# Kernel tuning notes

Measured on AMD Instinct MI355X. Metric: run time of the kernel, lower is better.

## Reference

```python
import jax, jax.numpy as jnp
from jax import lax
import numpy as np

B, N1, N2 = 4, 2048, 8192
C1, C2, K, F = 128, 64, 15, 128
NSAMPLE = 16
RADIUS = 0.2
KP_EXTEND = 1.0
EXTENT = KP_EXTEND * RADIUS  # area of influence of each kernel point


def setup_inputs() -> dict:
    key = jax.random.key(0)
    k0, k1, k2, k3, k4 = jax.random.split(key, 5)
    xyz1 = jax.random.uniform(k0, (B, N1, 3), dtype=jnp.float32)
    xyz2 = jax.random.uniform(k1, (B, N2, 3), dtype=jnp.float32)
    features1 = jax.random.normal(k2, (B, N1, C1), dtype=jnp.float32)
    features2 = jax.random.normal(k3, (B, N2, C2), dtype=jnp.float32)
    # Kernel points: fixed disposition inside a sphere of RADIUS, first point at
    # center (fixed='center'). Stands in for the offline potential-optimization.
    rng = np.random.RandomState(42)
    dirs = rng.randn(K, 3)
    dirs /= (np.linalg.norm(dirs, axis=1, keepdims=True) + 1e-9)
    rad = rng.rand(K, 1) ** (1.0 / 3.0)
    kp = dirs * rad
    kp[0, :] = 0.0  # fixed center point
    kernel_points = jnp.asarray(kp * RADIUS, dtype=jnp.float32)  # (K, 3)
    # Convolution kernel weights: one C1->F matrix per kernel point.
    W = jax.random.normal(k4, (K, C1, F), dtype=jnp.float32) * 0.05
    return {"xyz1": xyz1, "features1": features1, "xyz2": xyz2,
            "features2": features2, "kernel_points": kernel_points, "W": W}


def reference(xyz1, features1, xyz2, features2, kernel_points, W):
    # kNN search: for each query point in set 2, NSAMPLE nearest points in set 1.
    d2 = jnp.sum((xyz2[:, :, None, :] - xyz1[:, None, :, :]) ** 2, axis=-1)  # (B,N2,N1)
    _, idx = lax.top_k(-d2, NSAMPLE)  # (B, N2, S)
    # Irregular gather of neighbor coordinates and features.
    gather = jax.vmap(lambda arr, i: arr[i])  # per-batch fancy gather
    neigh_xyz = gather(xyz1, idx)        # (B, N2, S, 3)
    neigh_feat = gather(features1, idx)  # (B, N2, S, C1)
    # Neighbor positions relative to the query (center) point.
    rel = neigh_xyz - xyz2[:, :, None, :]  # (B, N2, S, 3)
    # Distances from each neighbor to each kernel point.
    diff = rel[:, :, :, None, :] - kernel_points[None, None, None, :, :]  # (B,N2,S,K,3)
    sq = jnp.sum(diff * diff, axis=-1)                                    # (B,N2,S,K)
    dist = jnp.sqrt(jnp.maximum(sq, 1e-12))
    # Linear kernel-point influence, aggregation_mode='sum'.
    weights = jax.nn.relu(1.0 - dist / EXTENT)  # (B, N2, S, K)
    # Weighted aggregation of neighbor features per kernel point.
    wf = jnp.einsum('bnsk,bnsc->bnkc', weights, neigh_feat)  # (B, N2, K, C1)
    # Kernel point convolution: per-kernel-point linear map, summed over K.
    out = jnp.einsum('bnkc,kcf->bnf', wf, W)  # (B, N2, F)
    out = jax.nn.relu(out)
    # Feature propagation: concat with skip features of set 2 (use_xyz=False).
    return jnp.concatenate([out, features2], axis=-1)  # (B, N2, F + C2)
```

## Files before the change

kernel.cpp:

```cpp
#include <hip/hip_runtime.h>

#define B 4
#define N1 2048
#define N2 8192
#define C1 128
#define C2 64
#define K 15
#define F 128
#define S 16

__global__ __launch_bounds__(512) void knn_kernel(
    const float* __restrict__ xyz1, const float* __restrict__ xyz2,
    unsigned short* __restrict__ nn_idx) {
#pragma clang fp contract(off)
  __shared__ float sx[N1], sy[N1], sz[N1];
  __shared__ float s_cd[16][522];
  __shared__ unsigned short s_ci[16][522];
  const int b = blockIdx.y;
  const int q0 = blockIdx.x * 16;
  const int tid = threadIdx.x;

  const float* p1 = xyz1 + (size_t)b * N1 * 3;
  for (int i = tid; i < N1; i += 512) {
    sx[i] = p1[i * 3 + 0];
    sy[i] = p1[i * 3 + 1];
    sz[i] = p1[i * 3 + 2];
  }
  __syncthreads();

  const int wv = tid >> 6;
  const int lane = tid & 63;
  const int q = lane & 15;
  const int sub = lane >> 4;
  const float* p2 = xyz2 + ((size_t)b * N2 + q0 + q) * 3;
  const float qx = p2[0], qy = p2[1], qz = p2[2];

  float bd[S];
  int bi[S];
#pragma unroll
  for (int j = 0; j < S; ++j) { bd[j] = 3.4e38f; bi[j] = 0x7fffffff; }

  const int i0 = wv * 256 + sub;
  for (int ii = 0; ii < 64; ++ii) {
    const int i = i0 + (ii << 2);
    float dx = qx - sx[i];
    float dy = qy - sy[i];
    float dz = qz - sz[i];
    float d = dx * dx;
    d = d + dy * dy;
    d = d + dz * dz;
    if (d < bd[S - 1]) {
      bd[S - 1] = d;
      bi[S - 1] = i;
#pragma unroll
      for (int j = S - 1; j > 0; --j) {
        if (bd[j] < bd[j - 1]) {
          float td = bd[j]; bd[j] = bd[j - 1]; bd[j - 1] = td;
          int ti = bi[j]; bi[j] = bi[j - 1]; bi[j - 1] = ti;
        }
      }
    }
  }
  {
    const int ls = (wv * 4 + sub) * 16;
#pragma unroll
    for (int j = 0; j < S; ++j) {
      s_cd[q][ls + j] = bd[j];
      s_ci[q][ls + j] = (unsigned short)bi[j];
    }
  }
  __syncthreads();

  for (int L = 32; L >= 4; L >>= 1) {
    const int half = L >> 1;
    const int nact = 16 * half;
    const int valid = tid < nact;
    float od[16];
    int oi[16];
    int q2 = 0, m = 0;
    if (valid) {
      q2 = tid / half;
      m = tid - q2 * half;
      int pa = (2 * m) * 16, ea = pa + 16;
      int pb = ea, eb = pb + 16;
#pragma unroll
      for (int j = 0; j < 16; ++j) {
        const int a_ok = pa < ea, b_ok = pb < eb;
        const int ra = a_ok ? pa : ea - 1;
        const int rb = b_ok ? pb : eb - 1;
        float da = s_cd[q2][ra];
        int ia = (int)s_ci[q2][ra];
        float db = s_cd[q2][rb];
        int ib = (int)s_ci[q2][rb];
        const int ta = a_ok && (!b_ok || da < db || (da == db && ia < ib));
        od[j] = ta ? da : db;
        oi[j] = ta ? ia : ib;
        pa += ta;
        pb += !ta;
      }
    }
    __syncthreads();
    if (valid) {
#pragma unroll
      for (int j = 0; j < 16; ++j) {
        s_cd[q2][m * 16 + j] = od[j];
        s_ci[q2][m * 16 + j] = (unsigned short)oi[j];
      }
    }
    __syncthreads();
  }

  if (tid < 16) {
    const int q2 = tid;
    int pa = 0, ea = 16, pb = 16, eb = 32;
    unsigned short* op = nn_idx + ((size_t)b * N2 + q0 + q2) * S;
#pragma unroll
    for (int j = 0; j < 16; ++j) {
      const int a_ok = pa < ea, b_ok = pb < eb;
      const int ra = a_ok ? pa : ea - 1;
      const int rb = b_ok ? pb : eb - 1;
      float da = s_cd[q2][ra];
      int ia = (int)s_ci[q2][ra];
      float db = s_cd[q2][rb];
      int ib = (int)s_ci[q2][rb];
      const int ta = a_ok && (!b_ok || da < db || (da == db && ia < ib));
      op[j] = (unsigned short)(ta ? ia : ib);
      pa += ta;
      pb += !ta;
    }
  }
}

__global__ __launch_bounds__(256) void conv_kernel(
    const float* __restrict__ xyz1, const float* __restrict__ feat1,
    const float* __restrict__ xyz2, const float* __restrict__ feat2,
    const float* __restrict__ kp, const float* __restrict__ W,
    const unsigned short* __restrict__ nn_idx, float* __restrict__ out) {
  __shared__ __align__(16) float s_buf[5184];
  int (*s_idx)[S] = (int(*)[S])(s_buf);
  float (*s_rel)[S][3] = (float(*)[S][3])(s_buf + 256);
  float (*s_w)[260] = (float(*)[260])(s_buf + 1024);
  float (*s_red)[16][132] = (float(*)[16][132])(s_buf);
  __shared__ float s_wf[C1][20];
  __shared__ float s_kp[K * 3];

  const int b = blockIdx.y;
  const int q0 = blockIdx.x * 16;
  const int tid = threadIdx.x;

  if (tid < K * 3) s_kp[tid] = kp[tid];
  s_idx[tid >> 4][tid & 15] = (int)nn_idx[((size_t)b * N2 + q0) * S + tid];
  __syncthreads();

  {
    int q = tid >> 4, s = tid & 15;
    int i = s_idx[q][s];
    const float* pn = xyz1 + ((size_t)b * N1 + i) * 3;
    const float* pq = xyz2 + ((size_t)b * N2 + q0 + q) * 3;
    s_rel[q][s][0] = pn[0] - pq[0];
    s_rel[q][s][1] = pn[1] - pq[1];
    s_rel[q][s][2] = pn[2] - pq[2];
  }
  __syncthreads();

  for (int t = tid; t < 16 * S * K; t += 256) {
    int q = t / (S * K);
    int r = t - q * (S * K);
    int s = r / K;
    int k = r - s * K;
    float rx = s_rel[q][s][0] - s_kp[k * 3 + 0];
    float ry = s_rel[q][s][1] - s_kp[k * 3 + 1];
    float rz = s_rel[q][s][2] - s_kp[k * 3 + 2];
    float d = sqrtf(fmaxf(rx * rx + ry * ry + rz * rz, 1e-12f));
    s_w[q][s * 16 + k] = fmaxf(0.0f, 1.0f - d / 0.2f);
  }
  __syncthreads();

  const int q = tid & 15;
  const int cg = tid >> 4;

  float wfr[K][8];
#pragma unroll
  for (int k = 0; k < K; ++k)
#pragma unroll
    for (int j = 0; j < 8; ++j) wfr[k][j] = 0.0f;

  for (int s = 0; s < S; ++s) {
    int i = s_idx[q][s];
    const float4* fp = (const float4*)(feat1 + ((size_t)b * N1 + i) * C1) + cg * 2;
    float4 n0 = fp[0];
    float4 n1 = fp[1];
    const float4* wr = (const float4*)(&s_w[q][s * 16]);
    float4 w0 = wr[0], w1 = wr[1], w2 = wr[2], w3 = wr[3];
    float wk[16] = {w0.x, w0.y, w0.z, w0.w, w1.x, w1.y, w1.z, w1.w,
                    w2.x, w2.y, w2.z, w2.w, w3.x, w3.y, w3.z, w3.w};
#pragma unroll
    for (int k = 0; k < K; ++k) {
      float w = wk[k];
      wfr[k][0] += w * n0.x;
      wfr[k][1] += w * n0.y;
      wfr[k][2] += w * n0.z;
      wfr[k][3] += w * n0.w;
      wfr[k][4] += w * n1.x;
      wfr[k][5] += w * n1.y;
      wfr[k][6] += w * n1.z;
      wfr[k][7] += w * n1.w;
    }
  }

  const int qg = tid >> 7;
  const int cs = (tid >> 5) & 3;
  const int fg = tid & 31;
  float4 acc[8];
#pragma unroll
  for (int qi = 0; qi < 8; ++qi) acc[qi] = make_float4(0.f, 0.f, 0.f, 0.f);

  for (int k = 0; k < K; ++k) {
    __syncthreads();
#pragma unroll
    for (int j = 0; j < 8; ++j) s_wf[cg * 8 + j][q] = wfr[k][j];
    __syncthreads();

    const float4* Wk4 = (const float4*)(W + (size_t)k * C1 * F) + fg;
#pragma unroll 4
    for (int c2 = 0; c2 < 32; ++c2) {
      int c = cs * 32 + c2;
      float4 wa = *(const float4*)(&s_wf[c][qg * 8 + 0]);
      float4 wb = *(const float4*)(&s_wf[c][qg * 8 + 4]);
      float4 w4 = Wk4[c * 32];
      acc[0].x += wa.x * w4.x; acc[0].y += wa.x * w4.y;
      acc[0].z += wa.x * w4.z; acc[0].w += wa.x * w4.w;
      acc[1].x += wa.y * w4.x; acc[1].y += wa.y * w4.y;
      acc[1].z += wa.y * w4.z; acc[1].w += wa.y * w4.w;
      acc[2].x += wa.z * w4.x; acc[2].y += wa.z * w4.y;
      acc[2].z += wa.z * w4.z; acc[2].w += wa.z * w4.w;
      acc[3].x += wa.w * w4.x; acc[3].y += wa.w * w4.y;
      acc[3].z += wa.w * w4.z; acc[3].w += wa.w * w4.w;
      acc[4].x += wb.x * w4.x; acc[4].y += wb.x * w4.y;
      acc[4].z += wb.x * w4.z; acc[4].w += wb.x * w4.w;
      acc[5].x += wb.y * w4.x; acc[5].y += wb.y * w4.y;
      acc[5].z += wb.y * w4.z; acc[5].w += wb.y * w4.w;
      acc[6].x += wb.z * w4.x; acc[6].y += wb.z * w4.y;
      acc[6].z += wb.z * w4.z; acc[6].w += wb.z * w4.w;
      acc[7].x += wb.w * w4.x; acc[7].y += wb.w * w4.y;
      acc[7].z += wb.w * w4.z; acc[7].w += wb.w * w4.w;
    }
  }

  const int qq0 = tid >> 5;
  const int qq1 = 8 + (tid >> 5);
  const int fj = tid & 31;

  if (cs < 2) {
#pragma unroll
    for (int qi = 0; qi < 8; ++qi)
      *(float4*)(&s_red[cs][qg * 8 + qi][fg * 4]) = acc[qi];
  }
  __syncthreads();

  float4 s01_0, s01_1;
  {
    float4 a0 = *(const float4*)&s_red[0][qq0][fj * 4];
    float4 a1 = *(const float4*)&s_red[1][qq0][fj * 4];
    s01_0.x = a0.x + a1.x; s01_0.y = a0.y + a1.y;
    s01_0.z = a0.z + a1.z; s01_0.w = a0.w + a1.w;
    float4 b0 = *(const float4*)&s_red[0][qq1][fj * 4];
    float4 b1 = *(const float4*)&s_red[1][qq1][fj * 4];
    s01_1.x = b0.x + b1.x; s01_1.y = b0.y + b1.y;
    s01_1.z = b0.z + b1.z; s01_1.w = b0.w + b1.w;
  }
  __syncthreads();
  if (cs >= 2) {
#pragma unroll
    for (int qi = 0; qi < 8; ++qi)
      *(float4*)(&s_red[cs - 2][qg * 8 + qi][fg * 4]) = acc[qi];
  }
  __syncthreads();
  {
    float4 a2 = *(const float4*)&s_red[0][qq0][fj * 4];
    float4 a3 = *(const float4*)&s_red[1][qq0][fj * 4];
    float4 v;
    v.x = fmaxf((s01_0.x + a2.x) + a3.x, 0.0f);
    v.y = fmaxf((s01_0.y + a2.y) + a3.y, 0.0f);
    v.z = fmaxf((s01_0.z + a2.z) + a3.z, 0.0f);
    v.w = fmaxf((s01_0.w + a2.w) + a3.w, 0.0f);
    ((float4*)(out + ((size_t)b * N2 + q0 + qq0) * (F + C2)))[fj] = v;
    float4 b2 = *(const float4*)&s_red[0][qq1][fj * 4];
    float4 b3 = *(const float4*)&s_red[1][qq1][fj * 4];
    float4 u;
    u.x = fmaxf((s01_1.x + b2.x) + b3.x, 0.0f);
    u.y = fmaxf((s01_1.y + b2.y) + b3.y, 0.0f);
    u.z = fmaxf((s01_1.z + b2.z) + b3.z, 0.0f);
    u.w = fmaxf((s01_1.w + b2.w) + b3.w, 0.0f);
    ((float4*)(out + ((size_t)b * N2 + q0 + qq1) * (F + C2)))[fj] = u;
  }

  {
    int qq = tid >> 4;
    int j = tid & 15;
    float4 v = ((const float4*)(feat2 + ((size_t)b * N2 + q0 + qq) * C2))[j];
    ((float4*)(out + ((size_t)b * N2 + q0 + qq) * (F + C2) + F))[j] = v;
  }
}

extern "C" void kernel_launch(void* const* d_in, const int* in_sizes, int n_in,
                              void* d_out, int out_size, void* d_ws, size_t ws_size,
                              hipStream_t stream) {
  const float* xyz1 = (const float*)d_in[0];
  const float* feat1 = (const float*)d_in[1];
  const float* xyz2 = (const float*)d_in[2];
  const float* feat2 = (const float*)d_in[3];
  const float* kp = (const float*)d_in[4];
  const float* Wm = (const float*)d_in[5];
  float* out = (float*)d_out;

  unsigned short* nn_idx = (unsigned short*)d_ws;

  knn_kernel<<<dim3(N2 / 16, B), 512, 0, stream>>>(xyz1, xyz2, nn_idx);
  conv_kernel<<<dim3(N2 / 16, B), 256, 0, stream>>>(xyz1, feat1, xyz2, feat2,
                                                    kp, Wm, nn_idx, out);
}
```

Before: 542.5 us.

## Split conv channel dimension into two halves to cut register pressure

The per-thread weighted-feature accumulator is split so each thread holds 15x4 values instead of 15x8, and the C1 channels are processed in two sequential halves of 64. Each half redoes the neighbor aggregation and then the K-loop GEMM into shared accumulators, with a sched_barrier between the halves. This is meant to lower VGPR usage and raise occupancy, and it also halves the s_wf shared buffer. The cost is twice as many K-loop syncthreads and repeated reads of the neighbor weights and indices.

```diff
diff --git a/kernel.cpp b/kernel.cpp
--- a/kernel.cpp
+++ b/kernel.cpp
@@ -141,7 +141,7 @@
   float (*s_rel)[S][3] = (float(*)[S][3])(s_buf + 256);
   float (*s_w)[260] = (float(*)[260])(s_buf + 1024);
   float (*s_red)[16][132] = (float(*)[16][132])(s_buf);
-  __shared__ float s_wf[C1][20];
+  __shared__ float s_wf[64][20];
   __shared__ float s_kp[K * 3];
 
   const int b = blockIdx.y;
@@ -178,72 +178,128 @@
 
   const int q = tid & 15;
   const int cg = tid >> 4;
-
-  float wfr[K][8];
-#pragma unroll
-  for (int k = 0; k < K; ++k)
-#pragma unroll
-    for (int j = 0; j < 8; ++j) wfr[k][j] = 0.0f;
-
-  for (int s = 0; s < S; ++s) {
-    int i = s_idx[q][s];
-    const float4* fp = (const float4*)(feat1 + ((size_t)b * N1 + i) * C1) + cg * 2;
-    float4 n0 = fp[0];
-    float4 n1 = fp[1];
-    const float4* wr = (const float4*)(&s_w[q][s * 16]);
-    float4 w0 = wr[0], w1 = wr[1], w2 = wr[2], w3 = wr[3];
-    float wk[16] = {w0.x, w0.y, w0.z, w0.w, w1.x, w1.y, w1.z, w1.w,
-                    w2.x, w2.y, w2.z, w2.w, w3.x, w3.y, w3.z, w3.w};
-#pragma unroll
-    for (int k = 0; k < K; ++k) {
-      float w = wk[k];
-      wfr[k][0] += w * n0.x;
-      wfr[k][1] += w * n0.y;
-      wfr[k][2] += w * n0.z;
-      wfr[k][3] += w * n0.w;
-      wfr[k][4] += w * n1.x;
-      wfr[k][5] += w * n1.y;
-      wfr[k][6] += w * n1.z;
-      wfr[k][7] += w * n1.w;
-    }
-  }
-
   const int qg = tid >> 7;
   const int cs = (tid >> 5) & 3;
   const int fg = tid & 31;
+
   float4 acc[8];
 #pragma unroll
   for (int qi = 0; qi < 8; ++qi) acc[qi] = make_float4(0.f, 0.f, 0.f, 0.f);
 
-  for (int k = 0; k < K; ++k) {
-    __syncthreads();
-#pragma unroll
-    for (int j = 0; j < 8; ++j) s_wf[cg * 8 + j][q] = wfr[k][j];
-    __syncthreads();
-
-    const float4* Wk4 = (const float4*)(W + (size_t)k * C1 * F) + fg;
+  {
+    float wfr[K][4];
+#pragma unroll
+    for (int k = 0; k < K; ++k)
+#pragma unroll
+      for (int j = 0; j < 4; ++j) wfr[k][j] = 0.0f;
+
+    for (int s = 0; s < S; ++s) {
+      int i = s_idx[q][s];
+      float4 n0 = *((const float4*)(feat1 + ((size_t)b * N1 + i) * C1) + cg);
+      const float4* wr = (const float4*)(&s_w[q][s * 16]);
+      float4 w0 = wr[0], w1 = wr[1], w2 = wr[2], w3 = wr[3];
+      float wk[16] = {w0.x, w0.y, w0.z, w0.w, w1.x, w1.y, w1.z, w1.w,
+                      w2.x, w2.y, w2.z, w2.w, w3.x, w3.y, w3.z, w3.w};
+#pragma unroll
+      for (int k = 0; k < K; ++k) {
+        float w = wk[k];
+        wfr[k][0] += w * n0.x;
+        wfr[k][1] += w * n0.y;
+        wfr[k][2] += w * n0.z;
+        wfr[k][3] += w * n0.w;
+      }
+    }
+
+    for (int k = 0; k < K; ++k) {
+      __syncthreads();
+#pragma unroll
+      for (int j = 0; j < 4; ++j) s_wf[cg * 4 + j][q] = wfr[k][j];
+      __syncthreads();
+
+      const float4* Wk4 = (const float4*)(W + (size_t)k * C1 * F) + fg;
 #pragma unroll 4
-    for (int c2 = 0; c2 < 32; ++c2) {
-      int c = cs * 32 + c2;
-      float4 wa = *(const float4*)(&s_wf[c][qg * 8 + 0]);
-      float4 wb = *(const float4*)(&s_wf[c][qg * 8 + 4]);
-      float4 w4 = Wk4[c * 32];
-      acc[0].x += wa.x * w4.x; acc[0].y += wa.x * w4.y;
-      acc[0].z += wa.x * w4.z; acc[0].w += wa.x * w4.w;
-      acc[1].x += wa.y * w4.x; acc[1].y += wa.y * w4.y;
-      acc[1].z += wa.y * w4.z; acc[1].w += wa.y * w4.w;
-      acc[2].x += wa.z * w4.x; acc[2].y += wa.z * w4.y;
-      acc[2].z += wa.z * w4.z; acc[2].w += wa.z * w4.w;
-      acc[3].x += wa.w * w4.x; acc[3].y += wa.w * w4.y;
-      acc[3].z += wa.w * w4.z; acc[3].w += wa.w * w4.w;
-      acc[4].x += wb.x * w4.x; acc[4].y += wb.x * w4.y;
-      acc[4].z += wb.x * w4.z; acc[4].w += wb.x * w4.w;
-      acc[5].x += wb.y * w4.x; acc[5].y += wb.y * w4.y;
-      acc[5].z += wb.y * w4.z; acc[5].w += wb.y * w4.w;
-      acc[6].x += wb.z * w4.x; acc[6].y += wb.z * w4.y;
-      acc[6].z += wb.z * w4.z; acc[6].w += wb.z * w4.w;
-      acc[7].x += wb.w * w4.x; acc[7].y += wb.w * w4.y;
-      acc[7].z += wb.w * w4.z; acc[7].w += wb.w * w4.w;
+      for (int c2 = 0; c2 < 16; ++c2) {
+        int cl = cs * 16 + c2;
+        float4 wa = *(const float4*)(&s_wf[cl][qg * 8 + 0]);
+        float4 wb = *(const float4*)(&s_wf[cl][qg * 8 + 4]);
+        float4 w4 = Wk4[cl * 32];
+        acc[0].x += wa.x * w4.x; acc[0].y += wa.x * w4.y;
+        acc[0].z += wa.x * w4.z; acc[0].w += wa.x * w4.w;
+        acc[1].x += wa.y * w4.x; acc[1].y += wa.y * w4.y;
+        acc[1].z += wa.y * w4.z; acc[1].w += wa.y * w4.w;
+        acc[2].x += wa.z * w4.x; acc[2].y += wa.z * w4.y;
+        acc[2].z += wa.z * w4.z; acc[2].w += wa.z * w4.w;
+        acc[3].x += wa.w * w4.x; acc[3].y += wa.w * w4.y;
+        acc[3].z += wa.w * w4.z; acc[3].w += wa.w * w4.w;
+        acc[4].x += wb.x * w4.x; acc[4].y += wb.x * w4.y;
+        acc[4].z += wb.x * w4.z; acc[4].w += wb.x * w4.w;
+        acc[5].x += wb.y * w4.x; acc[5].y += wb.y * w4.y;
+        acc[5].z += wb.y * w4.z; acc[5].w += wb.y * w4.w;
+        acc[6].x += wb.z * w4.x; acc[6].y += wb.z * w4.y;
+        acc[6].z += wb.z * w4.z; acc[6].w += wb.z * w4.w;
+        acc[7].x += wb.w * w4.x; acc[7].y += wb.w * w4.y;
+        acc[7].z += wb.w * w4.z; acc[7].w += wb.w * w4.w;
+      }
+    }
+  }
+
+  __builtin_amdgcn_sched_barrier(0);
+
+  {
+    float wfr[K][4];
+#pragma unroll
+    for (int k = 0; k < K; ++k)
+#pragma unroll
+      for (int j = 0; j < 4; ++j) wfr[k][j] = 0.0f;
+
+    for (int s = 0; s < S; ++s) {
+      int i = s_idx[q][s];
+      float4 n0 =
+          *((const float4*)(feat1 + ((size_t)b * N1 + i) * C1) + 16 + cg);
+      const float4* wr = (const float4*)(&s_w[q][s * 16]);
+      float4 w0 = wr[0], w1 = wr[1], w2 = wr[2], w3 = wr[3];
+      float wk[16] = {w0.x, w0.y, w0.z, w0.w, w1.x, w1.y, w1.z, w1.w,
+                      w2.x, w2.y, w2.z, w2.w, w3.x, w3.y, w3.z, w3.w};
+#pragma unroll
+      for (int k = 0; k < K; ++k) {
+        float w = wk[k];
+        wfr[k][0] += w * n0.x;
+        wfr[k][1] += w * n0.y;
+        wfr[k][2] += w * n0.z;
+        wfr[k][3] += w * n0.w;
+      }
+    }
+
+    for (int k = 0; k < K; ++k) {
+      __syncthreads();
+#pragma unroll
+      for (int j = 0; j < 4; ++j) s_wf[cg * 4 + j][q] = wfr[k][j];
+      __syncthreads();
+
+      const float4* Wk4 = (const float4*)(W + (size_t)k * C1 * F) + fg;
+#pragma unroll 4
+      for (int c2 = 0; c2 < 16; ++c2) {
+        int cl = cs * 16 + c2;
+        float4 wa = *(const float4*)(&s_wf[cl][qg * 8 + 0]);
+        float4 wb = *(const float4*)(&s_wf[cl][qg * 8 + 4]);
+        float4 w4 = Wk4[(64 + cl) * 32];
+        acc[0].x += wa.x * w4.x; acc[0].y += wa.x * w4.y;
+        acc[0].z += wa.x * w4.z; acc[0].w += wa.x * w4.w;
+        acc[1].x += wa.y * w4.x; acc[1].y += wa.y * w4.y;
+        acc[1].z += wa.y * w4.z; acc[1].w += wa.y * w4.w;
+        acc[2].x += wa.z * w4.x; acc[2].y += wa.z * w4.y;
+        acc[2].z += wa.z * w4.z; acc[2].w += wa.z * w4.w;
+        acc[3].x += wa.w * w4.x; acc[3].y += wa.w * w4.y;
+        acc[3].z += wa.w * w4.z; acc[3].w += wa.w * w4.w;
+        acc[4].x += wb.x * w4.x; acc[4].y += wb.x * w4.y;
+        acc[4].z += wb.x * w4.z; acc[4].w += wb.x * w4.w;
+        acc[5].x += wb.y * w4.x; acc[5].y += wb.y * w4.y;
+        acc[5].z += wb.y * w4.z; acc[5].w += wb.y * w4.w;
+        acc[6].x += wb.z * w4.x; acc[6].y += wb.z * w4.y;
+        acc[6].z += wb.z * w4.z; acc[6].w += wb.z * w4.w;
+        acc[7].x += wb.w * w4.x; acc[7].y += wb.w * w4.y;
+        acc[7].z += wb.w * w4.z; acc[7].w += wb.w * w4.w;
+      }
     }
   }
 
@@ -251,6 +307,7 @@
   const int qq1 = 8 + (tid >> 5);
   const int fj = tid & 31;
 
+  __syncthreads();
   if (cs < 2) {
 #pragma unroll
     for (int qi = 0; qi < 8; ++qi)
```

Result: slower. 864.0 us (+59.3%).
